# Performance work log

Hardware: AMD Instinct MI355X
Metric: run time of the kernel (lower is better)

## Reference

```python
import math
import jax, jax.numpy as jnp
import numpy as np

SCALES = [0.25, 1.0]


def _window_lengths(N):
    Ls = []
    for s in SCALES:
        Ls.append(int(math.floor(N * math.sqrt(s))))
        Ls.append(int(math.floor(N / math.sqrt(s))))
    return Ls


def _extract_windows(feature_seq, L):
    """feature_seq: (B, C, N) -> (B, N, C, L) windows centered at each position,
    zero-padded where the window extends outside [0, N)."""
    B, C, N = feature_seq.shape
    half = L // 2
    # idx[center, j] = center - half + j
    idx = jnp.arange(N)[:, None] - half + jnp.arange(L)[None, :]  # (N, L)
    valid = (idx >= 0) & (idx < N)
    gathered = feature_seq[:, :, jnp.clip(idx, 0, N - 1)]  # (B, C, N, L)
    gathered = jnp.where(valid[None, None, :, :], gathered, jnp.zeros((), feature_seq.dtype))
    return jnp.transpose(gathered, (0, 2, 1, 3))  # (B, N, C, L)


def setup_inputs() -> dict:
    key = jax.random.key(0)
    feature_seq = jax.random.normal(key, (2, 64, 512), dtype=jnp.float32)
    return {"feature_seq": feature_seq}


def reference(feature_seq):
    B, C, N = feature_seq.shape
    return tuple(_extract_windows(feature_seq, L) for L in _window_lengths(N))
```

## Files before the change

### kernel.cpp

```cpp
#include <hip/hip_runtime.h>


constexpr int B = 2;
constexpr int C = 64;
constexpr int N = 512;

constexpr int SZ256  = B * N * C * 256;
constexpr int SZ1024 = B * N * C * 1024;
constexpr int SZ512  = B * N * C * 512;

constexpr int BLK256  = SZ256  / 4 / 1024;
constexpr int BLK1024 = SZ1024 / 4 / 1024;
constexpr int BLK512  = SZ512  / 4 / 1024;
constexpr int NBLK = BLK256 + BLK1024 + 2 * BLK512;

typedef float f32x4 __attribute__((ext_vector_type(4)));

template <int L>
__device__ __forceinline__ void do_seg(const float* __restrict__ in,
                                       float* __restrict__ out,
                                       int blk, int tid) {
    constexpr int HALF = L / 2;
    constexpr int L4 = L / 4;
    constexpr int L4_BITS = (L == 256) ? 6 : (L == 512) ? 7 : 8;
    constexpr int KS = 256 >> L4_BITS;

    f32x4* __restrict__ out4 = reinterpret_cast<f32x4*>(out);

    const int l4    = tid & (L4 - 1);
    const int lb    = l4 << 2;
    const int restT = tid >> L4_BITS;
    const int R0    = (blk * 1024) >> L4_BITS;

#pragma unroll
    for (int k = 0; k < 4; ++k) {
        int t    = blk * 1024 + k * 256 + tid;
        int rest = R0 + k * KS + restT;

        int c  = rest & (C - 1);
        int bb = rest >> 15;
        int n  = (rest >> 6) & (N - 1);

        int roff = __builtin_amdgcn_readfirstlane((((bb << 6) | c) << 9));
        const float* __restrict__ row = in + roff;

        int idx = n - HALF + lb;

        f32x4 v;
        bool partial = ((idx > -4) && (idx < 0)) || ((idx > N - 4) && (idx < N));
        if (__any(partial)) {
            v.x = ((unsigned)(idx)     < (unsigned)N) ? row[idx]     : 0.0f;
            v.y = ((unsigned)(idx + 1) < (unsigned)N) ? row[idx + 1] : 0.0f;
            v.z = ((unsigned)(idx + 2) < (unsigned)N) ? row[idx + 2] : 0.0f;
            v.w = ((unsigned)(idx + 3) < (unsigned)N) ? row[idx + 3] : 0.0f;
        } else {
            __amdgpu_buffer_rsrc_t srd = __builtin_amdgcn_make_buffer_rsrc(
                (void*)row, (short)0,
                N * 4, 0x00020000);
            auto lv = __builtin_amdgcn_raw_buffer_load_b128(
                srd, (unsigned)(idx << 2), 0, 0);
            v = __builtin_bit_cast(f32x4, lv);
        }

        __builtin_nontemporal_store(v, out4 + t);
    }
}

__global__ __launch_bounds__(256)
void msw_fused_kernel(const float* __restrict__ in, float* __restrict__ out) {
    const int blk = blockIdx.x;
    const int tid = threadIdx.x;

    if (blk < BLK256) {
        do_seg<256>(in, out, blk, tid);
    } else if (blk < BLK256 + BLK1024) {
        do_seg<1024>(in, out + SZ256, blk - BLK256, tid);
    } else if (blk < BLK256 + BLK1024 + BLK512) {
        do_seg<512>(in, out + SZ256 + SZ1024, blk - (BLK256 + BLK1024), tid);
    } else {
        do_seg<512>(in, out + SZ256 + SZ1024 + SZ512,
                    blk - (BLK256 + BLK1024 + BLK512), tid);
    }
}

extern "C" void kernel_launch(void* const* d_in, const int* in_sizes, int n_in,
                              void* d_out, int out_size, void* d_ws, size_t ws_size,
                              hipStream_t stream) {
    const float* in = (const float*)d_in[0];
    float* out = (float*)d_out;

    msw_fused_kernel<<<NBLK, 256, 0, stream>>>(in, out);
}
```

Measured before the change: 119.0 us.

## Pre-pad input rows into workspace to remove bounds checks in window gather

Adds a small pre-pass kernel that copies each input row into a zero-padded 1536-float workspace row. The main kernel then reads every window chunk with a single unaligned vector load and needs no boundary checks, divergent scalar path, or buffer resource setup. In exchange it adds a second kernel launch with its own dependency, plus unaligned 16-byte loads. The kernel is bound by output writes, so the gain may be small.

```diff
diff --git a/kernel.cpp b/kernel.cpp
--- a/kernel.cpp
+++ b/kernel.cpp
@@ -14,21 +14,34 @@
 constexpr int BLK512  = SZ512  / 4 / 1024;
 constexpr int NBLK = BLK256 + BLK1024 + 2 * BLK512;
 
+constexpr int PROW = 1536;
+
 typedef float f32x4 __attribute__((ext_vector_type(4)));
+typedef float f32x4u __attribute__((ext_vector_type(4), aligned(4)));
+
+__global__ __launch_bounds__(384)
+void pad_kernel(const float* __restrict__ in, float* __restrict__ ws) {
+    const int row = blockIdx.x;
+    const int p = threadIdx.x;
+    f32x4 v = {0.0f, 0.0f, 0.0f, 0.0f};
+    if (p >= 128 && p < 256)
+        v = *reinterpret_cast<const f32x4*>(in + (row << 9) + ((p - 128) << 2));
+    *reinterpret_cast<f32x4*>(ws + row * PROW + (p << 2)) = v;
+}
 
 template <int L>
-__device__ __forceinline__ void do_seg(const float* __restrict__ in,
+__device__ __forceinline__ void do_seg(const float* __restrict__ ws,
                                        float* __restrict__ out,
                                        int blk, int tid) {
     constexpr int HALF = L / 2;
+    constexpr int BIAS = 512 - HALF;
     constexpr int L4 = L / 4;
     constexpr int L4_BITS = (L == 256) ? 6 : (L == 512) ? 7 : 8;
     constexpr int KS = 256 >> L4_BITS;
 
     f32x4* __restrict__ out4 = reinterpret_cast<f32x4*>(out);
 
-    const int l4    = tid & (L4 - 1);
-    const int lb    = l4 << 2;
+    const int lb    = (tid & (L4 - 1)) << 2;
     const int restT = tid >> L4_BITS;
     const int R0    = (blk * 1024) >> L4_BITS;
 
@@ -40,45 +53,28 @@
         int c  = rest & (C - 1);
         int bb = rest >> 15;
         int n  = (rest >> 6) & (N - 1);
+        int r  = (bb << 6) | c;
 
-        int roff = __builtin_amdgcn_readfirstlane((((bb << 6) | c) << 9));
-        const float* __restrict__ row = in + roff;
-
-        int idx = n - HALF + lb;
-
-        f32x4 v;
-        bool partial = ((idx > -4) && (idx < 0)) || ((idx > N - 4) && (idx < N));
-        if (__any(partial)) {
-            v.x = ((unsigned)(idx)     < (unsigned)N) ? row[idx]     : 0.0f;
-            v.y = ((unsigned)(idx + 1) < (unsigned)N) ? row[idx + 1] : 0.0f;
-            v.z = ((unsigned)(idx + 2) < (unsigned)N) ? row[idx + 2] : 0.0f;
-            v.w = ((unsigned)(idx + 3) < (unsigned)N) ? row[idx + 3] : 0.0f;
-        } else {
-            __amdgpu_buffer_rsrc_t srd = __builtin_amdgcn_make_buffer_rsrc(
-                (void*)row, (short)0,
-                N * 4, 0x00020000);
-            auto lv = __builtin_amdgcn_raw_buffer_load_b128(
-                srd, (unsigned)(idx << 2), 0, 0);
-            v = __builtin_bit_cast(f32x4, lv);
-        }
+        const float* __restrict__ src = ws + r * PROW + BIAS + n + lb;
+        f32x4 v = *reinterpret_cast<const f32x4u*>(src);
 
         __builtin_nontemporal_store(v, out4 + t);
     }
 }
 
 __global__ __launch_bounds__(256)
-void msw_fused_kernel(const float* __restrict__ in, float* __restrict__ out) {
+void msw_fused_kernel(const float* __restrict__ ws, float* __restrict__ out) {
     const int blk = blockIdx.x;
     const int tid = threadIdx.x;
 
     if (blk < BLK256) {
-        do_seg<256>(in, out, blk, tid);
+        do_seg<256>(ws, out, blk, tid);
     } else if (blk < BLK256 + BLK1024) {
-        do_seg<1024>(in, out + SZ256, blk - BLK256, tid);
+        do_seg<1024>(ws, out + SZ256, blk - BLK256, tid);
     } else if (blk < BLK256 + BLK1024 + BLK512) {
-        do_seg<512>(in, out + SZ256 + SZ1024, blk - (BLK256 + BLK1024), tid);
+        do_seg<512>(ws, out + SZ256 + SZ1024, blk - (BLK256 + BLK1024), tid);
     } else {
-        do_seg<512>(in, out + SZ256 + SZ1024 + SZ512,
+        do_seg<512>(ws, out + SZ256 + SZ1024 + SZ512,
                     blk - (BLK256 + BLK1024 + BLK512), tid);
     }
 }
@@ -88,6 +84,8 @@
                               hipStream_t stream) {
     const float* in = (const float*)d_in[0];
     float* out = (float*)d_out;
+    float* ws = (float*)d_ws;
 
-    msw_fused_kernel<<<NBLK, 256, 0, stream>>>(in, out);
+    pad_kernel<<<B * C, 384, 0, stream>>>(in, ws);
+    msw_fused_kernel<<<NBLK, 256, 0, stream>>>(ws, out);
 }
```

Measured after the change: 114.3 us (median of 2 runs). 3.9% less time.
